# Performance work log

Hardware: AMD Instinct MI355X
Metric: run time of the kernel (lower is better)

Reference implementation:

```python
import jax, jax.numpy as jnp
import numpy as np

B, T, D, U = 2048, 200, 128, 128  # batch, history len, input dim, gru units


def setup_inputs() -> dict:
    key = jax.random.key(0)
    ks = jax.random.split(key, 5)
    s = 1.0 / np.sqrt(U + D)
    return {
        "history_state": jax.random.normal(ks[0], (B, T, D), jnp.float32),
        "attention_score": jax.random.uniform(ks[1], (B, T, 1), jnp.float32),
        "Wu": jax.random.normal(ks[2], (U + D, U), jnp.float32) * s,
        "bu": jnp.zeros((U,), jnp.float32),
        "Wr": jax.random.normal(ks[3], (U + D, U), jnp.float32) * s,
        "br": jnp.zeros((U,), jnp.float32),
        "Wh": jax.random.normal(ks[4], (D + U, U), jnp.float32) * s,
        "bh": jnp.zeros((U,), jnp.float32),
    }


def reference(history_state, attention_score, Wu, bu, Wr, br, Wh, bh):
    # time-major for scan: (T, B, ...)
    xs = jnp.swapaxes(history_state, 0, 1)       # (T, B, D)
    ats = jnp.swapaxes(attention_score, 0, 1)    # (T, B, 1)
    h0 = jnp.zeros((history_state.shape[0], Wu.shape[1]), history_state.dtype)

    def step(h, xa):
        x, a = xa
        hx = jnp.concatenate([h, x], axis=-1)                       # (B, U+D)
        u = jax.nn.sigmoid(hx @ Wu + bu)                            # update gate
        r = jax.nn.sigmoid(hx @ Wr + br)                            # reset gate
        hh = jnp.tanh(jnp.concatenate([x, r * h], axis=-1) @ Wh + bh)
        u = u * a                                                   # attention-modulated update
        h_new = u * hh + (1.0 - u) * h
        return h_new, None

    h_final, _ = jax.lax.scan(step, h0, (xs, ats))
    return h_final  # (B, U)
```

## Files before the change

kernel.cpp:

```cpp
#include <hip/hip_runtime.h>
#include <hip/hip_bf16.h>


#define T_LEN 200
#define D_DIM 128
#define U_DIM 128
#define BM    16
#define CH    24
#define KCS   136
#define XSTEP (16 * KCS)

typedef __attribute__((ext_vector_type(8))) short bf16x8;
typedef __attribute__((ext_vector_type(4))) float f32x4;
typedef __attribute__((ext_vector_type(4))) unsigned int uint4v;

static __device__ __forceinline__ unsigned short f2bf(float f) {
    unsigned int u = __builtin_bit_cast(unsigned int, f);
    u += 0x7fffu + ((u >> 16) & 1u);
    return (unsigned short)(u >> 16);
}
static __device__ __forceinline__ unsigned int pkbf2(float a, float b) {
    float2 t; t.x = a; t.y = b;
    __hip_bfloat162 v = __float22bfloat162_rn(t);
    unsigned int u; __builtin_memcpy(&u, &v, 4);
    return u;
}
static __device__ __forceinline__ uint4v pack8u(float4 lo, float4 hi) {
    uint4v v;
    v[0] = pkbf2(lo.x, lo.y); v[1] = pkbf2(lo.z, lo.w);
    v[2] = pkbf2(hi.x, hi.y); v[3] = pkbf2(hi.z, hi.w);
    return v;
}
static __device__ __forceinline__ float fast_exp2(float x) {
#if __has_builtin(__builtin_amdgcn_exp2f)
    return __builtin_amdgcn_exp2f(x);
#else
    return exp2f(x);
#endif
}
static __device__ __forceinline__ float fast_rcp(float x) {
#if __has_builtin(__builtin_amdgcn_rcpf)
    return __builtin_amdgcn_rcpf(x);
#else
    return 1.0f / x;
#endif
}

__global__ __launch_bounds__(512, 2)
void gru_scan_kernel(const float* __restrict__ X,
                     const float* __restrict__ Att,
                     const float* __restrict__ Wu, const float* __restrict__ bu,
                     const float* __restrict__ Wr, const float* __restrict__ br,
                     const float* __restrict__ Wh, const float* __restrict__ bh,
                     float* __restrict__ out)
{
    __shared__ __align__(16) unsigned short x_sm[CH * XSTEP];
    __shared__ __align__(16) unsigned short h_bf[XSTEP];
    __shared__ __align__(16) unsigned short rh_bf[XSTEP];
    __shared__ float a_sm[CH * BM];

    const int tid  = threadIdx.x;
    const int wave = tid >> 6;
    const int lane = tid & 63;
    const int q    = lane >> 4;
    const int ln   = lane & 15;
    const int b0   = blockIdx.x * BM;

    const float INVLN2 = 1.4426950408889634f;

    bf16x8 wu[8], wr[8], wh[8];
    f32x4 nbu, nbr, bh2;
    {
        const int tb = 16 * wave;
        const int c  = tb + ln;
        const f32x4 bu4 = *(const f32x4*)&bu[tb + 4 * q];
        const f32x4 br4 = *(const f32x4*)&br[tb + 4 * q];
        const f32x4 bh4 = *(const f32x4*)&bh[tb + 4 * q];
        #pragma unroll
        for (int r = 0; r < 4; ++r) {
            nbu[r] = -bu4[r] * INVLN2;
            nbr[r] = -br4[r] * INVLN2;
            bh2[r] = 2.0f * bh4[r] * INVLN2;
        }
        #pragma unroll
        for (int kt = 0; kt < 8; ++kt) {
            const int k0 = 32 * kt + 8 * q;
            bf16x8 vu, vr, vh;
            #pragma unroll
            for (int j = 0; j < 8; ++j) {
                vu[j] = (short)f2bf(Wu[(k0 + j) * U_DIM + c] * -INVLN2);
                vr[j] = (short)f2bf(Wr[(k0 + j) * U_DIM + c] * -INVLN2);
                vh[j] = (short)f2bf(Wh[(k0 + j) * U_DIM + c] * (2.0f * INVLN2));
            }
            wu[kt] = vu; wr[kt] = vr; wh[kt] = vh;
        }
    }

    float hreg[4] = {0.f, 0.f, 0.f, 0.f};

    {
        unsigned int* hz = (unsigned int*)h_bf;
        unsigned int* rz = (unsigned int*)rh_bf;
        for (int i = tid; i < XSTEP / 2; i += 512) { hz[i] = 0; rz[i] = 0; }
    }

    const int s2   = tid >> 8;
    const int srow = (tid >> 4) & 15;
    const int cs   = tid & 15;
    const float* xbase = X + (size_t)(b0 + srow) * T_LEN * D_DIM + cs * 8;

    int t0 = 0;
    for (int ch = 0; ch < (T_LEN + CH - 1) / CH; ++ch) {
        const int L = (t0 + CH <= T_LEN) ? CH : (T_LEN - t0);

        {
            float4 px[CH];
            #pragma unroll
            for (int w2 = 0; w2 < CH / 2; ++w2) {
                int t = t0 + 2 * w2 + s2;
                t = (t < T_LEN) ? t : (T_LEN - 1);
                const float* src = xbase + (size_t)t * D_DIM;
                px[2 * w2]     = *(const float4*)(src);
                px[2 * w2 + 1] = *(const float4*)(src + 4);
            }
            float a_px = 0.0f;
            if (tid < BM * CH) {
                int t = t0 + (tid >> 4);
                t = (t < T_LEN) ? t : (T_LEN - 1);
                a_px = Att[(size_t)(b0 + (tid & 15)) * T_LEN + t];
            }
            #pragma unroll
            for (int w2 = 0; w2 < CH / 2; ++w2) {
                const int s = 2 * w2 + s2;
                *(uint4v*)&x_sm[s * XSTEP + cs * KCS + srow * 8] =
                    pack8u(px[2 * w2], px[2 * w2 + 1]);
            }
            if (tid < BM * CH) a_sm[tid] = a_px;
        }
        __syncthreads();

        f32x4 acc_r, acc_u, acc_h;
        {
            bf16x8 xf[4];
            #pragma unroll
            for (int kt = 0; kt < 4; ++kt)
                xf[kt] = *(const bf16x8*)&x_sm[(4 * kt + q) * KCS + ln * 8];
            acc_r = nbr; acc_u = nbu; acc_h = bh2;
            #pragma unroll
            for (int kt = 0; kt < 4; ++kt) {
                acc_r = __builtin_amdgcn_mfma_f32_16x16x32_bf16(wr[kt + 4], xf[kt], acc_r, 0, 0, 0);
                acc_u = __builtin_amdgcn_mfma_f32_16x16x32_bf16(wu[kt + 4], xf[kt], acc_u, 0, 0, 0);
                acc_h = __builtin_amdgcn_mfma_f32_16x16x32_bf16(wh[kt],     xf[kt], acc_h, 0, 0, 0);
            }
        }

        for (int s = 0; s < L; ++s) {
            bf16x8 hf[4];
            #pragma unroll
            for (int kt = 0; kt < 4; ++kt)
                hf[kt] = *(const bf16x8*)&h_bf[(4 * kt + q) * KCS + ln * 8];
            const float a_att = a_sm[s * BM + ln];

            f32x4 ra = acc_r, rb = (f32x4)0.0f;
            ra = __builtin_amdgcn_mfma_f32_16x16x32_bf16(wr[0], hf[0], ra, 0, 0, 0);
            rb = __builtin_amdgcn_mfma_f32_16x16x32_bf16(wr[2], hf[2], rb, 0, 0, 0);
            ra = __builtin_amdgcn_mfma_f32_16x16x32_bf16(wr[1], hf[1], ra, 0, 0, 0);
            rb = __builtin_amdgcn_mfma_f32_16x16x32_bf16(wr[3], hf[3], rb, 0, 0, 0);
            #pragma unroll
            for (int kt = 0; kt < 4; ++kt)
                acc_u = __builtin_amdgcn_mfma_f32_16x16x32_bf16(wu[kt], hf[kt], acc_u, 0, 0, 0);

            {
                float rh[4];
                #pragma unroll
                for (int r = 0; r < 4; ++r) {
                    float zr = ra[r] + rb[r];
                    float rv = fast_rcp(1.0f + fast_exp2(zr));
                    rh[r] = rv * hreg[r];
                }
                uint2 wv; wv.x = pkbf2(rh[0], rh[1]); wv.y = pkbf2(rh[2], rh[3]);
                const int c8 = 2 * wave + (q >> 1);
                *(uint2*)&rh_bf[c8 * KCS + ln * 8 + (q & 1) * 4] = wv;
            }
            __syncthreads();

            bf16x8 rf[4];
            #pragma unroll
            for (int kt = 0; kt < 4; ++kt)
                rf[kt] = *(const bf16x8*)&rh_bf[(4 * kt + q) * KCS + ln * 8];

            float uq[4];
            #pragma unroll
            for (int r = 0; r < 4; ++r) {
                float u = fast_rcp(1.0f + fast_exp2(acc_u[r]));
                uq[r] = u * a_att;
            }

            f32x4 ha = acc_h, hb = (f32x4)0.0f;
            ha = __builtin_amdgcn_mfma_f32_16x16x32_bf16(wh[4], rf[0], ha, 0, 0, 0);
            hb = __builtin_amdgcn_mfma_f32_16x16x32_bf16(wh[6], rf[2], hb, 0, 0, 0);
            ha = __builtin_amdgcn_mfma_f32_16x16x32_bf16(wh[5], rf[1], ha, 0, 0, 0);
            hb = __builtin_amdgcn_mfma_f32_16x16x32_bf16(wh[7], rf[3], hb, 0, 0, 0);

            #pragma unroll
            for (int r = 0; r < 4; ++r) {
                float z  = ha[r] + hb[r];
                float hh = 1.0f - 2.0f * fast_rcp(1.0f + fast_exp2(z));
                float ho = hreg[r];
                hreg[r] = ho + uq[r] * (hh - ho);
            }
            {
                uint2 wv; wv.x = pkbf2(hreg[0], hreg[1]); wv.y = pkbf2(hreg[2], hreg[3]);
                const int c8 = 2 * wave + (q >> 1);
                *(uint2*)&h_bf[c8 * KCS + ln * 8 + (q & 1) * 4] = wv;
            }

            if (s + 1 < L) {
                bf16x8 xf[4];
                #pragma unroll
                for (int kt = 0; kt < 4; ++kt)
                    xf[kt] = *(const bf16x8*)&x_sm[(s + 1) * XSTEP + (4 * kt + q) * KCS + ln * 8];
                acc_r = nbr; acc_u = nbu; acc_h = bh2;
                #pragma unroll
                for (int kt = 0; kt < 4; ++kt) {
                    acc_r = __builtin_amdgcn_mfma_f32_16x16x32_bf16(wr[kt + 4], xf[kt], acc_r, 0, 0, 0);
                    acc_u = __builtin_amdgcn_mfma_f32_16x16x32_bf16(wu[kt + 4], xf[kt], acc_u, 0, 0, 0);
                    acc_h = __builtin_amdgcn_mfma_f32_16x16x32_bf16(wh[kt],     xf[kt], acc_h, 0, 0, 0);
                }
            }
            __syncthreads();
        }
        t0 += CH;
    }

    {
        f32x4 v;
        #pragma unroll
        for (int r = 0; r < 4; ++r) v[r] = hreg[r];
        *(f32x4*)&out[(size_t)(b0 + ln) * U_DIM + 16 * wave + 4 * q] = v;
    }
}

extern "C" void kernel_launch(void* const* d_in, const int* in_sizes, int n_in,
                              void* d_out, int out_size, void* d_ws, size_t ws_size,
                              hipStream_t stream) {
    const float* X   = (const float*)d_in[0];
    const float* Att = (const float*)d_in[1];
    const float* Wu  = (const float*)d_in[2];
    const float* bu  = (const float*)d_in[3];
    const float* Wr  = (const float*)d_in[4];
    const float* br  = (const float*)d_in[5];
    const float* Wh  = (const float*)d_in[6];
    const float* bh  = (const float*)d_in[7];
    float* out = (float*)d_out;

    gru_scan_kernel<<<dim3(2048 / BM), dim3(512), 0, stream>>>(
        X, Att, Wu, bu, Wr, br, Wh, bh, out);
}
```

Baseline: 465.9 us.

## Prefetch next x chunk into registers during recurrence, lighten barriers

Global loads for the next time chunk of inputs and attention are now issued before the serial recurrence over the current chunk and written to shared memory afterwards, so HBM latency overlaps compute instead of stalling each chunk. The chunk size is halved to keep the prefetch registers affordable, and launch bounds drop to one block per SM-equivalent occupancy hint. In-loop __syncthreads are replaced with an explicit LDS waitcnt plus s_barrier. The trade-off is more chunk iterations and possibly lower occupancy, which reduces latency hiding across blocks.

```diff
diff --git a/kernel.cpp b/kernel.cpp
--- a/kernel.cpp
+++ b/kernel.cpp
@@ -6,13 +6,16 @@
 #define D_DIM 128
 #define U_DIM 128
 #define BM    16
-#define CH    24
+#define CH    12
+#define NCH   ((T_LEN + CH - 1) / CH)
 #define KCS   136
 #define XSTEP (16 * KCS)
 
 typedef __attribute__((ext_vector_type(8))) short bf16x8;
 typedef __attribute__((ext_vector_type(4))) float f32x4;
 typedef __attribute__((ext_vector_type(4))) unsigned int uint4v;
+
+#define MFMA __builtin_amdgcn_mfma_f32_16x16x32_bf16
 
 static __device__ __forceinline__ unsigned short f2bf(float f) {
     unsigned int u = __builtin_bit_cast(unsigned int, f);
@@ -45,8 +48,14 @@
     return 1.0f / x;
 #endif
 }
-
-__global__ __launch_bounds__(512, 2)
+static __device__ __forceinline__ void block_sync_lds() {
+    asm volatile("s_waitcnt lgkmcnt(0)" ::: "memory");
+    __builtin_amdgcn_sched_barrier(0);
+    __builtin_amdgcn_s_barrier();
+    __builtin_amdgcn_sched_barrier(0);
+}
+
+__global__ __launch_bounds__(512, 1)
 void gru_scan_kernel(const float* __restrict__ X,
                      const float* __restrict__ Att,
                      const float* __restrict__ Wu, const float* __restrict__ bu,
@@ -109,35 +118,51 @@
     const int cs   = tid & 15;
     const float* xbase = X + (size_t)(b0 + srow) * T_LEN * D_DIM + cs * 8;
 
+    {
+        float4 p0[CH];
+        #pragma unroll
+        for (int w2 = 0; w2 < CH / 2; ++w2) {
+            const int t = 2 * w2 + s2;
+            const float* src = xbase + (size_t)t * D_DIM;
+            p0[2 * w2]     = *(const float4*)(src);
+            p0[2 * w2 + 1] = *(const float4*)(src + 4);
+        }
+        float a_px = 0.0f;
+        if (tid < BM * CH)
+            a_px = Att[(size_t)(b0 + (tid & 15)) * T_LEN + (tid >> 4)];
+        #pragma unroll
+        for (int w2 = 0; w2 < CH / 2; ++w2) {
+            const int s = 2 * w2 + s2;
+            *(uint4v*)&x_sm[s * XSTEP + cs * KCS + srow * 8] =
+                pack8u(p0[2 * w2], p0[2 * w2 + 1]);
+        }
+        if (tid < BM * CH) a_sm[tid] = a_px;
+    }
+    __syncthreads();
+
     int t0 = 0;
-    for (int ch = 0; ch < (T_LEN + CH - 1) / CH; ++ch) {
-        const int L = (t0 + CH <= T_LEN) ? CH : (T_LEN - t0);
-
-        {
-            float4 px[CH];
+    for (int ch = 0; ch < NCH; ++ch) {
+        const int L  = (t0 + CH <= T_LEN) ? CH : (T_LEN - t0);
+        const bool st = (ch + 1 < NCH);
+
+        float4 px[CH];
+        float av = 0.0f;
+        if (st) {
+            const int tn0 = t0 + CH;
             #pragma unroll
             for (int w2 = 0; w2 < CH / 2; ++w2) {
-                int t = t0 + 2 * w2 + s2;
+                int t = tn0 + 2 * w2 + s2;
                 t = (t < T_LEN) ? t : (T_LEN - 1);
                 const float* src = xbase + (size_t)t * D_DIM;
                 px[2 * w2]     = *(const float4*)(src);
                 px[2 * w2 + 1] = *(const float4*)(src + 4);
             }
-            float a_px = 0.0f;
             if (tid < BM * CH) {
-                int t = t0 + (tid >> 4);
-                t = (t < T_LEN) ? t : (T_LEN - 1);
-                a_px = Att[(size_t)(b0 + (tid & 15)) * T_LEN + t];
-            }
-            #pragma unroll
-            for (int w2 = 0; w2 < CH / 2; ++w2) {
-                const int s = 2 * w2 + s2;
-                *(uint4v*)&x_sm[s * XSTEP + cs * KCS + srow * 8] =
-                    pack8u(px[2 * w2], px[2 * w2 + 1]);
-            }
-            if (tid < BM * CH) a_sm[tid] = a_px;
-        }
-        __syncthreads();
+                int ta = tn0 + (tid >> 4);
+                ta = (ta < T_LEN) ? ta : (T_LEN - 1);
+                av = Att[(size_t)(b0 + (tid & 15)) * T_LEN + ta];
+            }
+        }
 
         f32x4 acc_r, acc_u, acc_h;
         {
@@ -148,9 +173,9 @@
             acc_r = nbr; acc_u = nbu; acc_h = bh2;
             #pragma unroll
             for (int kt = 0; kt < 4; ++kt) {
-                acc_r = __builtin_amdgcn_mfma_f32_16x16x32_bf16(wr[kt + 4], xf[kt], acc_r, 0, 0, 0);
-                acc_u = __builtin_amdgcn_mfma_f32_16x16x32_bf16(wu[kt + 4], xf[kt], acc_u, 0, 0, 0);
-                acc_h = __builtin_amdgcn_mfma_f32_16x16x32_bf16(wh[kt],     xf[kt], acc_h, 0, 0, 0);
+                acc_r = MFMA(wr[kt + 4], xf[kt], acc_r, 0, 0, 0);
+                acc_u = MFMA(wu[kt + 4], xf[kt], acc_u, 0, 0, 0);
+                acc_h = MFMA(wh[kt],     xf[kt], acc_h, 0, 0, 0);
             }
         }
 
@@ -162,13 +187,13 @@
             const float a_att = a_sm[s * BM + ln];
 
             f32x4 ra = acc_r, rb = (f32x4)0.0f;
-            ra = __builtin_amdgcn_mfma_f32_16x16x32_bf16(wr[0], hf[0], ra, 0, 0, 0);
-            rb = __builtin_amdgcn_mfma_f32_16x16x32_bf16(wr[2], hf[2], rb, 0, 0, 0);
-            ra = __builtin_amdgcn_mfma_f32_16x16x32_bf16(wr[1], hf[1], ra, 0, 0, 0);
-            rb = __builtin_amdgcn_mfma_f32_16x16x32_bf16(wr[3], hf[3], rb, 0, 0, 0);
-            #pragma unroll
-            for (int kt = 0; kt < 4; ++kt)
-                acc_u = __builtin_amdgcn_mfma_f32_16x16x32_bf16(wu[kt], hf[kt], acc_u, 0, 0, 0);
+            ra = MFMA(wr[0], hf[0], ra, 0, 0, 0);
+            rb = MFMA(wr[2], hf[2], rb, 0, 0, 0);
+            ra = MFMA(wr[1], hf[1], ra, 0, 0, 0);
+            rb = MFMA(wr[3], hf[3], rb, 0, 0, 0);
+            #pragma unroll
+            for (int kt = 0; kt < 4; ++kt)
+                acc_u = MFMA(wu[kt], hf[kt], acc_u, 0, 0, 0);
 
             {
                 float rh[4];
@@ -182,7 +207,7 @@
                 const int c8 = 2 * wave + (q >> 1);
                 *(uint2*)&rh_bf[c8 * KCS + ln * 8 + (q & 1) * 4] = wv;
             }
-            __syncthreads();
+            block_sync_lds();
 
             bf16x8 rf[4];
             #pragma unroll
@@ -197,10 +222,10 @@
             }
 
             f32x4 ha = acc_h, hb = (f32x4)0.0f;
-            ha = __builtin_amdgcn_mfma_f32_16x16x32_bf16(wh[4], rf[0], ha, 0, 0, 0);
-            hb = __builtin_amdgcn_mfma_f32_16x16x32_bf16(wh[6], rf[2], hb, 0, 0, 0);
-            ha = __builtin_amdgcn_mfma_f32_16x16x32_bf16(wh[5], rf[1], ha, 0, 0, 0);
-            hb = __builtin_amdgcn_mfma_f32_16x16x32_bf16(wh[7], rf[3], hb, 0, 0, 0);
+            ha = MFMA(wh[4], rf[0], ha, 0, 0, 0);
+            hb = MFMA(wh[6], rf[2], hb, 0, 0, 0);
+            ha = MFMA(wh[5], rf[1], ha, 0, 0, 0);
+            hb = MFMA(wh[7], rf[3], hb, 0, 0, 0);
 
             #pragma unroll
             for (int r = 0; r < 4; ++r) {
@@ -223,11 +248,22 @@
                 acc_r = nbr; acc_u = nbu; acc_h = bh2;
                 #pragma unroll
                 for (int kt = 0; kt < 4; ++kt) {
-                    acc_r = __builtin_amdgcn_mfma_f32_16x16x32_bf16(wr[kt + 4], xf[kt], acc_r, 0, 0, 0);
-                    acc_u = __builtin_amdgcn_mfma_f32_16x16x32_bf16(wu[kt + 4], xf[kt], acc_u, 0, 0, 0);
-                    acc_h = __builtin_amdgcn_mfma_f32_16x16x32_bf16(wh[kt],     xf[kt], acc_h, 0, 0, 0);
+                    acc_r = MFMA(wr[kt + 4], xf[kt], acc_r, 0, 0, 0);
+                    acc_u = MFMA(wu[kt + 4], xf[kt], acc_u, 0, 0, 0);
+                    acc_h = MFMA(wh[kt],     xf[kt], acc_h, 0, 0, 0);
                 }
             }
+            block_sync_lds();
+        }
+
+        if (st) {
+            #pragma unroll
+            for (int w2 = 0; w2 < CH / 2; ++w2) {
+                const int s = 2 * w2 + s2;
+                *(uint4v*)&x_sm[s * XSTEP + cs * KCS + srow * 8] =
+                    pack8u(px[2 * w2], px[2 * w2 + 1]);
+            }
+            if (tid < BM * CH) a_sm[tid] = av;
             __syncthreads();
         }
         t0 += CH;
```

Result: faster. 452.9 us (-2.8%).
